# Optimization experiments

Measured on AMD Instinct MI355X. Metric: run time of the kernel, lower is better.

The kernel has to match this reference:

```python
import jax, jax.numpy as jnp
import numpy as np
import math

D_MODEL, D_HEAD = 1024, 64
N_HEADS = D_MODEL // D_HEAD  # 16
EPS = 1e-6

def rms_norm(x, scale, eps=EPS):
    ms = jnp.mean(x * x, axis=-1, keepdims=True)
    return x * scale * jax.lax.rsqrt(ms + eps)

def apply_rotary_emb(x, theta):
    # theta: (..., d) rotates first 2*d dims of x
    d = theta.shape[-1]
    x1, x2, x3 = x[..., :d], x[..., d:2 * d], x[..., 2 * d:]
    cos, sin = jnp.cos(theta), jnp.sin(theta)
    return jnp.concatenate([x1 * cos - x2 * sin, x2 * cos + x1 * sin, x3], axis=-1)

def make_freqs():
    d4 = D_HEAD // 4  # 16
    log_min, log_max = math.log(math.pi), math.log(10.0 * math.pi)
    f = np.exp(np.linspace(log_min, log_max, N_HEADS * d4 + 1, dtype=np.float64)[:-1])
    return jnp.asarray(f.reshape(d4, N_HEADS).T, dtype=jnp.float32)  # (n_heads, d_head//4)

def setup_inputs() -> dict:
    key = jax.random.key(0)
    ks = jax.random.split(key, 8)
    n, l = 4, 1024
    x = jax.random.normal(ks[0], (n, l, D_MODEL), jnp.float32)
    pos = jax.random.uniform(ks[1], (n, l, 2), jnp.float32)
    attn_mask = jnp.ones((1, 1, l, l), dtype=bool)
    cond = jax.random.normal(ks[2], (n, 1, D_MODEL), jnp.float32)
    norm_w = jax.random.normal(ks[3], (D_MODEL, D_MODEL), jnp.float32) * 0.02
    qkv_w = jax.random.normal(ks[4], (3 * D_MODEL, D_MODEL), jnp.float32) * (D_MODEL ** -0.5)
    qk_scale = jnp.ones((N_HEADS, 1, 1), jnp.float32)
    out_w = jax.random.normal(ks[5], (D_MODEL, D_MODEL), jnp.float32) * 0.02
    freqs = make_freqs()
    return {"x": x, "pos": pos, "attn_mask": attn_mask, "cond": cond,
            "norm_w": norm_w, "qkv_w": qkv_w, "qk_scale": qk_scale,
            "freqs": freqs, "out_w": out_w}

def reference(x, pos, attn_mask, cond, norm_w, qkv_w, qk_scale, freqs, out_w):
    n, l, d = x.shape
    # AdaRMSNorm
    h = rms_norm(x, jnp.einsum('nlc,dc->nld', cond, norm_w) + 1.0)
    # QKV projection -> (n, h, l, e)
    qkv = jnp.einsum('nld,ed->nle', h, qkv_w)
    q, k, v = jnp.split(qkv, 3, axis=-1)
    split_heads = lambda t: t.reshape(n, l, N_HEADS, D_HEAD).transpose(0, 2, 1, 3)
    q, k, v = split_heads(q), split_heads(k), split_heads(v)
    # per-head RMSNorm (scale shape (h,1,1))
    q = rms_norm(q, qk_scale)
    k = rms_norm(k, qk_scale)
    # axial RoPE: theta (n, h, l, d_head//2)
    theta = jnp.concatenate([
        pos[:, None, :, 0:1] * freqs[None, :, None, :],
        pos[:, None, :, 1:2] * freqs[None, :, None, :],
    ], axis=-1)
    q = apply_rotary_emb(q, theta)
    k = apply_rotary_emb(k, theta)
    # SDPA
    scores = jnp.einsum('nhqe,nhke->nhqk', q, k) * (D_HEAD ** -0.5)
    scores = jnp.where(attn_mask, scores, jnp.float32(-1e30))
    attn = jax.nn.softmax(scores, axis=-1)
    o = jnp.einsum('nhqk,nhke->nhqe', attn, v)
    o = o.transpose(0, 2, 1, 3).reshape(n, l, d)
    return jnp.einsum('nld,ed->nle', o, out_w)
```

## Files before the change

kernel.cpp:

```cpp
#include <hip/hip_runtime.h>

typedef short bf16x8 __attribute__((ext_vector_type(8)));
typedef float f32x4 __attribute__((ext_vector_type(4)));

__device__ __forceinline__ float bf2f(ushort u) {
  union { unsigned int i; float f; } x; x.i = ((unsigned int)u) << 16; return x.f;
}
__device__ __forceinline__ ushort f2bf(float f) {
  union { float f; unsigned int i; } x; x.f = f;
  unsigned int r = x.i + 0x7fff + ((x.i >> 16) & 1);
  return (ushort)(r >> 16);
}
__device__ __forceinline__ unsigned int cvtpk_bf16(float a, float b) {
  unsigned int r;
  asm("v_cvt_pk_bf16_f32 %0, %1, %2" : "=v"(r) : "v"(a), "v"(b));
  return r;
}

__device__ __forceinline__ f32x4 mfma16(bf16x8 a, bf16x8 b, f32x4 c) {
  return __builtin_amdgcn_mfma_f32_16x16x32_bf16(a, b, c, 0, 0, 0);
}

__device__ __forceinline__ void gload_lds16(const void* g, void* l) {
  __builtin_amdgcn_global_load_lds(
      (const __attribute__((address_space(1))) void*)g,
      (__attribute__((address_space(3))) void*)l, 16, 0, 0);
}

__global__ __launch_bounds__(256) void prep0(
    const float* __restrict__ qkv_w, ushort* __restrict__ qkvw_bf,
    const float* __restrict__ out_w, ushort* __restrict__ outw_bf,
    const float* __restrict__ cond, const float* __restrict__ nw,
    float* __restrict__ sout) {
  const int b = blockIdx.x;
  if (b < 4096) {
    const float* src;
    ushort* dst;
    int j;
    if (b < 3072) {
      src = qkv_w; dst = qkvw_bf; j = b * 256 + threadIdx.x;
    } else {
      src = out_w; dst = outw_bf; j = (b - 3072) * 256 + threadIdx.x;
    }
    float4 v = ((const float4*)src)[j];
    ushort4 o;
    o.x = f2bf(v.x); o.y = f2bf(v.y); o.z = f2bf(v.z); o.w = f2bf(v.w);
    ((ushort4*)dst)[j] = o;
    return;
  }
  const int w = threadIdx.x >> 6, lane = threadIdx.x & 63;
  const int idx = (b - 4096) * 4 + w;
  const int n_ = idx >> 10, d = idx & 1023;
  const float* cr = cond + n_ * 1024;
  const float* wr_ = nw + (size_t)d * 1024;
  float sum = 0.f;
#pragma unroll
  for (int c = lane; c < 1024; c += 64) sum += cr[c] * wr_[c];
#pragma unroll
  for (int off = 1; off < 64; off <<= 1) sum += __shfl_xor(sum, off);
  if (lane == 0) sout[idx] = sum + 1.0f;
}

__global__ __launch_bounds__(256) void rmsnorm_x(const float* __restrict__ x,
                                                 const float* __restrict__ s,
                                                 ushort* __restrict__ h, int L) {
  const int row = blockIdx.x;
  const int n_ = row / L;
  const int tid = threadIdx.x;
  __shared__ float red[4];
  float4 xv = ((const float4*)(x + (size_t)row * 1024))[tid];
  float ss = xv.x * xv.x + xv.y * xv.y + xv.z * xv.z + xv.w * xv.w;
#pragma unroll
  for (int off = 1; off < 64; off <<= 1) ss += __shfl_xor(ss, off);
  if ((tid & 63) == 0) red[tid >> 6] = ss;
  __syncthreads();
  float tot = red[0] + red[1] + red[2] + red[3];
  float r = rsqrtf(tot * (1.f / 1024.f) + 1e-6f);
  float4 sv = ((const float4*)(s + (size_t)n_ * 1024))[tid];
  ushort4 o;
  o.x = f2bf(xv.x * sv.x * r);
  o.y = f2bf(xv.y * sv.y * r);
  o.z = f2bf(xv.z * sv.z * r);
  o.w = f2bf(xv.w * sv.w * r);
  ((ushort4*)(h + (size_t)row * 1024))[tid] = o;
}

template <typename OT>
__global__ __launch_bounds__(256) void gemm_bt(const ushort* __restrict__ A,
                                               const ushort* __restrict__ B,
                                               OT* __restrict__ C, int M, int N,
                                               int K, int nbx) {
  __shared__ ushort As[2][128 * 32];
  __shared__ ushort Bs[2][128 * 32];
  const int tid = threadIdx.x;
  const int w = tid >> 6;
  const int lane = tid & 63;
  const int wr = w >> 1, wc = w & 1;
  const int lm = lane & 15, g = lane >> 4;
  const int qchunk = gridDim.x >> 3;
  const int swz = (blockIdx.x & 7) * qchunk + (blockIdx.x >> 3);
  const int bn = (swz % nbx) * 128;
  const int bm = (swz / nbx) * 128;
  f32x4 acc[4][4] = {};
  const int u_ = lane >> 3;
  const int pp = (lane & 7) ^ u_;
  const int srow = (u_ << 1) | (pp >> 2);
  const int scol = (pp & 3) * 8;
  const int rb = (lm >> 1) * 64 + (((((lm & 1) << 2) | g) ^ (lm >> 1)) << 3);

  auto stage = [&](int kt, int b) {
#pragma unroll
    for (int i = 0; i < 2; ++i) {
      const int c = w * 2 + i;
      gload_lds16(&A[(size_t)(bm + c * 16 + srow) * K + kt + scol],
                  &As[b][c * 512]);
      gload_lds16(&B[(size_t)(bn + c * 16 + srow) * K + kt + scol],
                  &Bs[b][c * 512]);
    }
  };

  const int NTK = K >> 5;
  stage(0, 0);
  stage(32, 1);
  for (int t = 0; t < NTK; ++t) {
    const int b = t & 1;
    if (t + 1 < NTK)
      asm volatile("s_waitcnt vmcnt(4)" ::: "memory");
    else
      asm volatile("s_waitcnt vmcnt(0)" ::: "memory");
    __builtin_amdgcn_s_barrier();
    bf16x8 af[4], bfr[4];
#pragma unroll
    for (int mi = 0; mi < 4; ++mi)
      af[mi] = *(const bf16x8*)&As[b][(wr * 4 + mi) * 512 + rb];
#pragma unroll
    for (int ni = 0; ni < 4; ++ni)
      bfr[ni] = *(const bf16x8*)&Bs[b][(wc * 4 + ni) * 512 + rb];
    asm volatile("s_waitcnt lgkmcnt(0)" ::: "memory");
    __builtin_amdgcn_sched_barrier(0);
    __builtin_amdgcn_s_barrier();
    if (t + 2 < NTK) stage((t + 2) << 5, b);
#pragma unroll
    for (int mi = 0; mi < 4; ++mi)
#pragma unroll
      for (int ni = 0; ni < 4; ++ni)
        acc[mi][ni] = mfma16(af[mi], bfr[ni], acc[mi][ni]);
  }
#pragma unroll
  for (int mi = 0; mi < 4; ++mi)
#pragma unroll
    for (int ni = 0; ni < 4; ++ni) {
      int col = bn + wc * 64 + ni * 16 + lm;
#pragma unroll
      for (int r = 0; r < 4; ++r) {
        int row = bm + wr * 64 + mi * 16 + g * 4 + r;
        float v = acc[mi][ni][r];
        if constexpr (sizeof(OT) == 2)
          C[(size_t)row * N + col] = (OT)f2bf(v);
        else
          C[(size_t)row * N + col] = (OT)v;
      }
    }
}

__global__ __launch_bounds__(256) void qkv_prep_t(
    const ushort* __restrict__ qkv, const float* __restrict__ pos,
    const float* __restrict__ qscale, const float* __restrict__ freqs,
    ushort* __restrict__ Qr, ushort* __restrict__ Kr, ushort* __restrict__ Vt,
    int L) {
  __shared__ ushort T[64][72];
  const int tid = threadIdx.x;
  const int w = tid >> 6, lane = tid & 63;
  const int bid = blockIdx.x;
  const int nh = bid >> 4;
  const int lc = bid & 15;
  const int n_ = nh >> 4, h = nh & 15;
  const int l0 = lc * 64;
  const float sc = qscale[h];
  const int tl = lane & 31;
  const float fr = freqs[h * 16 + (tl & 15)];
#pragma unroll
  for (int i = 0; i < 16; ++i) {
    const int r = i * 4 + w;
    const int row = n_ * L + l0 + r;
    const size_t ib = (size_t)row * 3072 + h * 64 + lane;
    float qv = bf2f(qkv[ib]);
    float kv = bf2f(qkv[ib + 1024]);
    float vv = bf2f(qkv[ib + 2048]);
    float sq = qv * qv, sk = kv * kv;
#pragma unroll
    for (int off = 1; off < 64; off <<= 1) {
      sq += __shfl_xor(sq, off);
      sk += __shfl_xor(sk, off);
    }
    float qn = qv * sc * rsqrtf(sq * (1.f / 64.f) + 1e-6f);
    float kn = kv * sc * rsqrtf(sk * (1.f / 64.f) + 1e-6f);
    const float p0 = pos[row * 2 + 0], p1 = pos[row * 2 + 1];
    float th = ((tl < 16) ? p0 : p1) * fr;
    float s_, c_;
    sincosf(th, &s_, &c_);
    float qo = __shfl_xor(qn, 32);
    float ko = __shfl_xor(kn, 32);
    float qr = (lane < 32) ? (qn * c_ - qo * s_) : (qn * c_ + qo * s_);
    float kr = (lane < 32) ? (kn * c_ - ko * s_) : (kn * c_ + ko * s_);
    const size_t ob = ((size_t)nh * L + l0 + r) * 64 + lane;
    Qr[ob] = f2bf(qr * 0.18033688f);
    Kr[ob] = f2bf(kr);
    T[r][lane] = f2bf(vv);
  }
  __syncthreads();
  const int d = tid >> 2;
  const int lc4 = (tid & 3) * 16;
  ushort tmp[16];
#pragma unroll
  for (int j = 0; j < 16; ++j) tmp[j] = T[lc4 + j][d];
  ushort* dst = Vt + ((size_t)nh * 64 + d) * L + l0 + lc4;
  *(uint4*)dst = *(uint4*)&tmp[0];
  *(uint4*)(dst + 8) = *(uint4*)&tmp[8];
}

__global__ __launch_bounds__(256) void attn_kernel(
    const ushort* __restrict__ Q, const ushort* __restrict__ Kg,
    const ushort* __restrict__ Vtg, ushort* __restrict__ O, int L) {
  __shared__ ushort Ks[2][64 * 64];
  __shared__ ushort Vs[2][64 * 64];
  __shared__ ushort Pb[4][32 * 64];
  const int tid = threadIdx.x;
  const int w = tid >> 6, lane = tid & 63;
  const int lm = lane & 15, g = lane >> 4;
  const int swz = (blockIdx.x & 7) * 64 + (blockIdx.x >> 3);
  const int nh = swz >> 3;
  const int qt = swz & 7;
  const ushort* q = Q + (size_t)nh * L * 64;
  const ushort* k = Kg + (size_t)nh * L * 64;
  const ushort* vt = Vtg + (size_t)nh * 64 * L;
  const int qbase = qt * 128 + w * 32;
  bf16x8 qf[2][2];
#pragma unroll
  for (int qs = 0; qs < 2; ++qs)
#pragma unroll
    for (int kc = 0; kc < 2; ++kc)
      qf[qs][kc] = *(const bf16x8*)&q[(size_t)(qbase + qs * 16 + lm) * 64 +
                                      kc * 32 + g * 8];
  f32x4 ot[2][4] = {};
  f32x4 lsacc[2] = {};
  bf16x8 ones;
#pragma unroll
  for (int i = 0; i < 8; ++i) ones[i] = (short)0x3F80;
  const int sr = lane >> 3;
  const int ss = (lane & 7) ^ sr;

  auto stage = [&](int tt, int b) {
#pragma unroll
    for (int i = 0; i < 2; ++i) {
      const int r = w * 16 + i * 8 + sr;
      gload_lds16(&k[(size_t)(tt * 64 + r) * 64 + ss * 8],
                  &Ks[b][(w * 16 + i * 8) * 64]);
    }
#pragma unroll
    for (int i = 0; i < 2; ++i) {
      const int r = w * 16 + i * 8 + sr;
      gload_lds16(&vt[(size_t)r * L + tt * 64 + ss * 8],
                  &Vs[b][(w * 16 + i * 8) * 64]);
    }
  };

  stage(0, 0);
  __syncthreads();
  const int NT = L >> 6;
  for (int t = 0; t < NT; ++t) {
    const int cur = t & 1;
    if (t + 1 < NT) stage(t + 1, cur ^ 1);
    const ushort* ksb = &Ks[cur][0];
    f32x4 st[2][4] = {};
    __builtin_amdgcn_s_setprio(1);
#pragma unroll
    for (int t16 = 0; t16 < 4; ++t16) {
      const int r = t16 * 16 + lm;
#pragma unroll
      for (int kc = 0; kc < 2; ++kc) {
        bf16x8 a = *(const bf16x8*)&ksb[r * 64 + (((kc * 4 + g) ^ (lm & 7)) << 3)];
        st[0][t16] = mfma16(a, qf[0][kc], st[0][t16]);
        st[1][t16] = mfma16(a, qf[1][kc], st[1][t16]);
      }
    }
    __builtin_amdgcn_s_setprio(0);
    float e[2][4][4];
#pragma unroll
    for (int qs = 0; qs < 2; ++qs)
#pragma unroll
      for (int t16 = 0; t16 < 4; ++t16)
#pragma unroll
        for (int r = 0; r < 4; ++r)
          e[qs][t16][r] = __builtin_amdgcn_exp2f(st[qs][t16][r]);
    ushort* pb = &Pb[w][0];
#pragma unroll
    for (int qs = 0; qs < 2; ++qs)
#pragma unroll
      for (int t16 = 0; t16 < 4; ++t16) {
        unsigned int lo = cvtpk_bf16(e[qs][t16][0], e[qs][t16][1]);
        unsigned int hi = cvtpk_bf16(e[qs][t16][2], e[qs][t16][3]);
        const int slot = (t16 * 2 + (g >> 1)) ^ (lm & 7);
        *(uint2*)&pb[(qs * 16 + lm) * 64 + slot * 8 + (g & 1) * 4] =
            make_uint2(lo, hi);
      }
    asm volatile("s_waitcnt lgkmcnt(0)" ::: "memory");
    __builtin_amdgcn_sched_barrier(0);
    bf16x8 pf[2][2];
#pragma unroll
    for (int qs = 0; qs < 2; ++qs)
#pragma unroll
      for (int c = 0; c < 2; ++c)
        pf[qs][c] = *(const bf16x8*)&pb[(qs * 16 + lm) * 64 +
                                        (((c * 4 + g) ^ (lm & 7)) << 3)];
    const ushort* vsb = &Vs[cur][0];
    __builtin_amdgcn_s_setprio(1);
#pragma unroll
    for (int db = 0; db < 4; ++db) {
      const int d = db * 16 + lm;
#pragma unroll
      for (int c = 0; c < 2; ++c) {
        bf16x8 a = *(const bf16x8*)&vsb[d * 64 + (((c * 4 + g) ^ (lm & 7)) << 3)];
        ot[0][db] = mfma16(a, pf[0][c], ot[0][db]);
        ot[1][db] = mfma16(a, pf[1][c], ot[1][db]);
      }
    }
#pragma unroll
    for (int qs = 0; qs < 2; ++qs)
#pragma unroll
      for (int c = 0; c < 2; ++c)
        lsacc[qs] = mfma16(ones, pf[qs][c], lsacc[qs]);
    __builtin_amdgcn_s_setprio(0);
    __syncthreads();
  }
  const int n_ = nh >> 4, h = nh & 15;
#pragma unroll
  for (int qs = 0; qs < 2; ++qs) {
    const float inv = 1.f / lsacc[qs][0];
#pragma unroll
    for (int db = 0; db < 4; ++db) {
      unsigned int lo = cvtpk_bf16(ot[qs][db][0] * inv, ot[qs][db][1] * inv);
      unsigned int hi = cvtpk_bf16(ot[qs][db][2] * inv, ot[qs][db][3] * inv);
      size_t off = ((size_t)(n_ * L + qbase + qs * 16 + lm) * 1024) + h * 64 +
                   db * 16 + g * 4;
      *(uint2*)&O[off] = make_uint2(lo, hi);
    }
  }
}

extern "C" void kernel_launch(void* const* d_in, const int* in_sizes, int n_in,
                              void* d_out, int out_size, void* d_ws,
                              size_t ws_size, hipStream_t stream) {
  const float* x = (const float*)d_in[0];
  const float* pos = (const float*)d_in[1];
  const float* cond = (const float*)d_in[3];
  const float* norm_w = (const float*)d_in[4];
  const float* qkv_w = (const float*)d_in[5];
  const float* qk_scale = (const float*)d_in[6];
  const float* freqs = (const float*)d_in[7];
  const float* out_w = (const float*)d_in[8];
  float* out = (float*)d_out;
  const int L = 1024;

  char* wsb = (char*)d_ws;
  ushort* qkvw_bf = (ushort*)(wsb);
  ushort* outw_bf = (ushort*)(wsb + 6291456);
  float* s_cond = (float*)(wsb + 8388608);
  ushort* h_buf = (ushort*)(wsb + 8404992);
  ushort* qkv_buf = (ushort*)(wsb + 16793600);
  ushort* q_r = (ushort*)(wsb + 41959424);
  ushort* k_r = (ushort*)(wsb + 50348032);
  ushort* o_buf = (ushort*)(wsb + 67125248);
  ushort* vt_buf = h_buf;

  hipLaunchKernelGGL(prep0, dim3(5120), dim3(256), 0, stream, qkv_w, qkvw_bf,
                     out_w, outw_bf, cond, norm_w, s_cond);
  hipLaunchKernelGGL(rmsnorm_x, dim3(4096), dim3(256), 0, stream, x, s_cond,
                     h_buf, L);
  hipLaunchKernelGGL(gemm_bt<ushort>, dim3(768), dim3(256), 0, stream, h_buf,
                     qkvw_bf, qkv_buf, 4096, 3072, 1024, 24);
  hipLaunchKernelGGL(qkv_prep_t, dim3(1024), dim3(256), 0, stream, qkv_buf,
                     pos, qk_scale, freqs, q_r, k_r, vt_buf, L);
  hipLaunchKernelGGL(attn_kernel, dim3(512), dim3(256), 0, stream, q_r, k_r,
                     vt_buf, o_buf, L);
  hipLaunchKernelGGL(gemm_bt<float>, dim3(256), dim3(256), 0, stream, o_buf,
                     outw_bf, out, 4096, 1024, 1024, 8);
}
```

Before: 116.9 us.

## Software-pipeline attention loop: skew PV by one tile with triple-buffered K/V

Restructures the attention main loop so the P·V MFMAs for tile u-1 run in the same iteration as the QK^T and exp for tile u, with K staged two tiles ahead and V one tile ahead in triple-buffered LDS. Explicit vmcnt waits plus a single s_barrier replace the previous double-buffer __syncthreads scheme. The aim is to overlap the softmax/exp VALU work with matrix-core work and hide global-to-LDS load latency. In exchange it uses more LDS (about 16 KB extra), which may reduce occupancy, and adds hand-counted wait logic that must stay exact.

```diff
diff --git a/kernel.cpp b/kernel.cpp
--- a/kernel.cpp
+++ b/kernel.cpp
@@ -222,8 +222,8 @@
 __global__ __launch_bounds__(256) void attn_kernel(
     const ushort* __restrict__ Q, const ushort* __restrict__ Kg,
     const ushort* __restrict__ Vtg, ushort* __restrict__ O, int L) {
-  __shared__ ushort Ks[2][64 * 64];
-  __shared__ ushort Vs[2][64 * 64];
+  __shared__ ushort Ks[3][64 * 64];
+  __shared__ ushort Vs[3][64 * 64];
   __shared__ ushort Pb[4][32 * 64];
   const int tid = threadIdx.x;
   const int w = tid >> 6, lane = tid & 63;
@@ -250,88 +250,105 @@
   const int sr = lane >> 3;
   const int ss = (lane & 7) ^ sr;
 
-  auto stage = [&](int tt, int b) {
+  auto stageK = [&](int tt, int slot) {
 #pragma unroll
     for (int i = 0; i < 2; ++i) {
       const int r = w * 16 + i * 8 + sr;
       gload_lds16(&k[(size_t)(tt * 64 + r) * 64 + ss * 8],
-                  &Ks[b][(w * 16 + i * 8) * 64]);
-    }
+                  &Ks[slot][(w * 16 + i * 8) * 64]);
+    }
+  };
+  auto stageV = [&](int tt, int slot) {
 #pragma unroll
     for (int i = 0; i < 2; ++i) {
       const int r = w * 16 + i * 8 + sr;
       gload_lds16(&vt[(size_t)r * L + tt * 64 + ss * 8],
-                  &Vs[b][(w * 16 + i * 8) * 64]);
+                  &Vs[slot][(w * 16 + i * 8) * 64]);
     }
   };
 
-  stage(0, 0);
-  __syncthreads();
   const int NT = L >> 6;
-  for (int t = 0; t < NT; ++t) {
-    const int cur = t & 1;
-    if (t + 1 < NT) stage(t + 1, cur ^ 1);
-    const ushort* ksb = &Ks[cur][0];
-    f32x4 st[2][4] = {};
-    __builtin_amdgcn_s_setprio(1);
-#pragma unroll
-    for (int t16 = 0; t16 < 4; ++t16) {
-      const int r = t16 * 16 + lm;
-#pragma unroll
-      for (int kc = 0; kc < 2; ++kc) {
-        bf16x8 a = *(const bf16x8*)&ksb[r * 64 + (((kc * 4 + g) ^ (lm & 7)) << 3)];
-        st[0][t16] = mfma16(a, qf[0][kc], st[0][t16]);
-        st[1][t16] = mfma16(a, qf[1][kc], st[1][t16]);
+  stageK(0, 0);
+  stageK(1, 1);
+  stageV(0, 0);
+
+  bf16x8 pfp[2][2] = {};
+  for (int u = 0; u <= NT; ++u) {
+    if (u <= NT - 2)
+      asm volatile("s_waitcnt vmcnt(4)" ::: "memory");
+    else if (u == NT - 1)
+      asm volatile("s_waitcnt vmcnt(2)" ::: "memory");
+    else
+      asm volatile("s_waitcnt vmcnt(0)" ::: "memory");
+    __builtin_amdgcn_s_barrier();
+    if (u + 2 < NT) stageK(u + 2, (u + 2) % 3);
+    if (u + 1 < NT) stageV(u + 1, (u + 1) % 3);
+    float e[2][4][4];
+    if (u < NT) {
+      const ushort* ksb = &Ks[u % 3][0];
+      f32x4 st[2][4] = {};
+      __builtin_amdgcn_s_setprio(1);
+#pragma unroll
+      for (int t16 = 0; t16 < 4; ++t16) {
+        const int r = t16 * 16 + lm;
+#pragma unroll
+        for (int kc = 0; kc < 2; ++kc) {
+          bf16x8 a =
+              *(const bf16x8*)&ksb[r * 64 + (((kc * 4 + g) ^ (lm & 7)) << 3)];
+          st[0][t16] = mfma16(a, qf[0][kc], st[0][t16]);
+          st[1][t16] = mfma16(a, qf[1][kc], st[1][t16]);
+        }
       }
-    }
-    __builtin_amdgcn_s_setprio(0);
-    float e[2][4][4];
-#pragma unroll
-    for (int qs = 0; qs < 2; ++qs)
-#pragma unroll
-      for (int t16 = 0; t16 < 4; ++t16)
-#pragma unroll
-        for (int r = 0; r < 4; ++r)
-          e[qs][t16][r] = __builtin_amdgcn_exp2f(st[qs][t16][r]);
-    ushort* pb = &Pb[w][0];
-#pragma unroll
-    for (int qs = 0; qs < 2; ++qs)
-#pragma unroll
-      for (int t16 = 0; t16 < 4; ++t16) {
-        unsigned int lo = cvtpk_bf16(e[qs][t16][0], e[qs][t16][1]);
-        unsigned int hi = cvtpk_bf16(e[qs][t16][2], e[qs][t16][3]);
-        const int slot = (t16 * 2 + (g >> 1)) ^ (lm & 7);
-        *(uint2*)&pb[(qs * 16 + lm) * 64 + slot * 8 + (g & 1) * 4] =
-            make_uint2(lo, hi);
+      __builtin_amdgcn_s_setprio(0);
+#pragma unroll
+      for (int qs = 0; qs < 2; ++qs)
+#pragma unroll
+        for (int t16 = 0; t16 < 4; ++t16)
+#pragma unroll
+          for (int r = 0; r < 4; ++r)
+            e[qs][t16][r] = __builtin_amdgcn_exp2f(st[qs][t16][r]);
+      ushort* pb = &Pb[w][0];
+#pragma unroll
+      for (int qs = 0; qs < 2; ++qs)
+#pragma unroll
+        for (int t16 = 0; t16 < 4; ++t16) {
+          unsigned int lo = cvtpk_bf16(e[qs][t16][0], e[qs][t16][1]);
+          unsigned int hi = cvtpk_bf16(e[qs][t16][2], e[qs][t16][3]);
+          const int slot = (t16 * 2 + (g >> 1)) ^ (lm & 7);
+          *(uint2*)&pb[(qs * 16 + lm) * 64 + slot * 8 + (g & 1) * 4] =
+              make_uint2(lo, hi);
+        }
+    }
+    if (u > 0) {
+      const ushort* vsb = &Vs[(u - 1) % 3][0];
+#pragma unroll
+      for (int db = 0; db < 4; ++db) {
+        const int d = db * 16 + lm;
+#pragma unroll
+        for (int c = 0; c < 2; ++c) {
+          bf16x8 a =
+              *(const bf16x8*)&vsb[d * 64 + (((c * 4 + g) ^ (lm & 7)) << 3)];
+          ot[0][db] = mfma16(a, pfp[0][c], ot[0][db]);
+          ot[1][db] = mfma16(a, pfp[1][c], ot[1][db]);
+        }
       }
-    asm volatile("s_waitcnt lgkmcnt(0)" ::: "memory");
-    __builtin_amdgcn_sched_barrier(0);
-    bf16x8 pf[2][2];
-#pragma unroll
-    for (int qs = 0; qs < 2; ++qs)
-#pragma unroll
-      for (int c = 0; c < 2; ++c)
-        pf[qs][c] = *(const bf16x8*)&pb[(qs * 16 + lm) * 64 +
-                                        (((c * 4 + g) ^ (lm & 7)) << 3)];
-    const ushort* vsb = &Vs[cur][0];
-    __builtin_amdgcn_s_setprio(1);
-#pragma unroll
-    for (int db = 0; db < 4; ++db) {
-      const int d = db * 16 + lm;
-#pragma unroll
-      for (int c = 0; c < 2; ++c) {
-        bf16x8 a = *(const bf16x8*)&vsb[d * 64 + (((c * 4 + g) ^ (lm & 7)) << 3)];
-        ot[0][db] = mfma16(a, pf[0][c], ot[0][db]);
-        ot[1][db] = mfma16(a, pf[1][c], ot[1][db]);
-      }
-    }
-#pragma unroll
-    for (int qs = 0; qs < 2; ++qs)
-#pragma unroll
-      for (int c = 0; c < 2; ++c)
-        lsacc[qs] = mfma16(ones, pf[qs][c], lsacc[qs]);
-    __builtin_amdgcn_s_setprio(0);
-    __syncthreads();
+#pragma unroll
+      for (int qs = 0; qs < 2; ++qs)
+#pragma unroll
+        for (int c = 0; c < 2; ++c)
+          lsacc[qs] = mfma16(ones, pfp[qs][c], lsacc[qs]);
+    }
+    if (u < NT) {
+      asm volatile("s_waitcnt lgkmcnt(0)" ::: "memory");
+      __builtin_amdgcn_sched_barrier(0);
+      const ushort* pb = &Pb[w][0];
+#pragma unroll
+      for (int qs = 0; qs < 2; ++qs)
+#pragma unroll
+        for (int c = 0; c < 2; ++c)
+          pfp[qs][c] = *(const bf16x8*)&pb[(qs * 16 + lm) * 64 +
+                                           (((c * 4 + g) ^ (lm & 7)) << 3)];
+    }
   }
   const int n_ = nh >> 4, h = nh & 15;
 #pragma unroll
```

Result: no change. 118.3 us (+1.2%).
